# Performance work log

Measured on AMD Instinct MI355X. Metric: run time of the kernel, lower is better.

The kernel has to match this reference:

```python
import jax, jax.numpy as jnp
import numpy as np
import math

BSZ, SEQLEN, DIM = 16, 1, 4096
N_HEADS, N_KV_HEADS = 32, 8
HEAD_DIM = DIM // N_HEADS  # 128
MAX_SEQ_LEN = 4096
START_POS = 4095


def setup_inputs() -> dict:
    key = jax.random.key(0)
    ks = jax.random.split(key, 8)
    w_scale = 0.02
    x = jax.random.normal(ks[0], (1, BSZ, SEQLEN, DIM), jnp.float32)
    wq = jax.random.normal(ks[1], (DIM, DIM), jnp.float32) * w_scale
    wk = jax.random.normal(ks[2], (N_KV_HEADS * HEAD_DIM, DIM), jnp.float32) * w_scale
    wv = jax.random.normal(ks[3], (N_KV_HEADS * HEAD_DIM, DIM), jnp.float32) * w_scale
    wo = jax.random.normal(ks[4], (DIM, DIM), jnp.float32) * w_scale
    cache_k = jax.random.normal(ks[5], (BSZ, MAX_SEQ_LEN, N_KV_HEADS, HEAD_DIM), jnp.float32)
    cache_v = jax.random.normal(ks[6], (BSZ, MAX_SEQ_LEN, N_KV_HEADS, HEAD_DIM), jnp.float32)
    # real RoPE frequencies for positions [START_POS, START_POS+SEQLEN)
    inv_freq = 1.0 / (10000.0 ** (np.arange(0, HEAD_DIM, 2, dtype=np.float32) / HEAD_DIM))
    pos = np.arange(START_POS, START_POS + SEQLEN, dtype=np.float32)
    ang = pos[:, None] * inv_freq[None, :]  # [seqlen, head_dim/2]
    freqs_cos = jnp.asarray(np.cos(ang), jnp.float32)
    freqs_sin = jnp.asarray(np.sin(ang), jnp.float32)
    return {"x": x, "wq": wq, "wk": wk, "wv": wv, "wo": wo,
            "cache_k": cache_k, "cache_v": cache_v,
            "freqs_cos": freqs_cos, "freqs_sin": freqs_sin,
            "start_pos": START_POS}


def _apply_rope(t, cos, sin):
    # t: [b, s, h, d]; cos/sin: [s, d/2]; complex mult over interleaved pairs
    b, s, h, d = t.shape
    tr = t.reshape(b, s, h, d // 2, 2)
    a, bb = tr[..., 0], tr[..., 1]
    c = cos[None, :, None, :]
    sn = sin[None, :, None, :]
    out = jnp.stack([a * c - bb * sn, a * sn + bb * c], axis=-1)
    return out.reshape(b, s, h, d)


def reference(x, wq, wk, wv, wo, cache_k, cache_v, freqs_cos, freqs_sin, start_pos):
    _, bsz, seqlen, dim = x.shape
    n_kv_heads, head_dim = cache_k.shape[2], cache_k.shape[3]
    n_heads = dim // head_dim
    n_rep = n_heads // n_kv_heads

    xq = jnp.einsum('obsd,ed->obse', x, wq).reshape(bsz, seqlen, n_heads, head_dim)
    xk = jnp.einsum('obsd,ed->obse', x, wk).reshape(bsz, seqlen, n_kv_heads, head_dim)
    xv = jnp.einsum('obsd,ed->obse', x, wv).reshape(bsz, seqlen, n_kv_heads, head_dim)

    xq = _apply_rope(xq, freqs_cos, freqs_sin)
    xk = _apply_rope(xk, freqs_cos, freqs_sin)

    cache_k = cache_k.at[:, start_pos:start_pos + seqlen].set(xk)
    cache_v = cache_v.at[:, start_pos:start_pos + seqlen].set(xv)
    keys = cache_k[:, :start_pos + seqlen]    # [b, L, kvh, hd]
    values = cache_v[:, :start_pos + seqlen]

    # repeat_kv (GQA expansion)
    keys = jnp.repeat(keys, n_rep, axis=2)     # [b, L, h, hd]
    values = jnp.repeat(values, n_rep, axis=2)

    scale = 1.0 / math.sqrt(head_dim)
    scores = jnp.einsum('bqhd,bkhd->bhqk', xq, keys) * scale
    # mask is None in decode (seqlen == 1)
    attn = jax.nn.softmax(scores, axis=-1)
    out = jnp.einsum('bhqk,bkhd->bqhd', attn, values)
    out = out.reshape(1, bsz, seqlen, dim)
    return jnp.einsum('obsd,ed->obse', out, wo)
```

## Files before the change

kernel.cpp:

```cpp
#include <hip/hip_runtime.h>
#include <math.h>

#define BSZ 16
#define DIMM 4096
#define NKVH 8
#define HD 128
#define SEQ 4096
#define NSPLIT 16
#define SPLITLEN 256
#define RPAD 65

__device__ __forceinline__ void gemv_rows2(const float* __restrict__ xg,
                                           const float* __restrict__ W,
                                           int rbase,
                                           float* __restrict__ x_lds,
                                           float* __restrict__ rbuf,
                                           float res[2], int tid) {
  const int lane = tid & 63;
  float acc[2][16];
#pragma unroll
  for (int r = 0; r < 2; ++r)
#pragma unroll
    for (int b = 0; b < 16; ++b) acc[r][b] = 0.f;

  for (int c = 0; c < 16; ++c) {
    __syncthreads();
#pragma unroll
    for (int u = 0; u < 4; ++u) {
      int f = u * 256 + tid;
      int b = f >> 6;
      int dl = (f & 63) << 2;
      ((float4*)x_lds)[f] = *(const float4*)(xg + (size_t)b * DIMM + c * 256 + dl);
    }
    __syncthreads();
    float4 w4[2];
#pragma unroll
    for (int r = 0; r < 2; ++r)
      w4[r] = *(const float4*)(W + (size_t)(rbase + r) * DIMM + c * 256 + (lane << 2));
#pragma unroll
    for (int b = 0; b < 16; ++b) {
      float4 xv = ((const float4*)x_lds)[b * 64 + lane];
#pragma unroll
      for (int r = 0; r < 2; ++r) {
        acc[r][b] = fmaf(w4[r].x, xv.x, acc[r][b]);
        acc[r][b] = fmaf(w4[r].y, xv.y, acc[r][b]);
        acc[r][b] = fmaf(w4[r].z, xv.z, acc[r][b]);
        acc[r][b] = fmaf(w4[r].w, xv.w, acc[r][b]);
      }
    }
  }
#pragma unroll
  for (int r = 0; r < 2; ++r) {
    __syncthreads();
#pragma unroll
    for (int b = 0; b < 16; ++b) rbuf[b * RPAD + lane] = acc[r][b];
    __syncthreads();
    int bb = lane >> 2, j = lane & 3;
    float s = 0.f;
#pragma unroll
    for (int k = 0; k < 16; ++k) s += rbuf[bb * RPAD + j * 16 + k];
    s += __shfl_xor(s, 1);
    s += __shfl_xor(s, 2);
    res[r] = s;
  }
}

__global__ __launch_bounds__(256) void qkv_kernel(
    const float* __restrict__ x, const float* __restrict__ wq,
    const float* __restrict__ wk, const float* __restrict__ wv,
    const float* __restrict__ fcos, const float* __restrict__ fsin,
    float* __restrict__ q_ws, float* __restrict__ ckw, float* __restrict__ cvw) {
  __shared__ float x_lds[4096];
  __shared__ float red[4][16 * RPAD];
  const int tid = threadIdx.x;
  const int lane = tid & 63;
  const int wave = tid >> 6;
  const int row0 = blockIdx.x * 8 + wave * 2;

  const float* W;
  int rbase, kind;
  if (row0 < 4096)      { W = wq; rbase = row0;        kind = 0; }
  else if (row0 < 5120) { W = wk; rbase = row0 - 4096; kind = 1; }
  else                  { W = wv; rbase = row0 - 5120; kind = 2; }

  float res[2];
  gemv_rows2(x, W, rbase, x_lds, red[wave], res, tid);

  if (kind <= 1) {
    int i = (rbase & 127) >> 1;
    float c = fcos[i], s = fsin[i];
    float a = res[0], b2 = res[1];
    res[0] = a * c - b2 * s;
    res[1] = a * s + b2 * c;
  }
  if ((lane & 3) == 0) {
    int b = lane >> 2;
    if (kind == 0) {
#pragma unroll
      for (int r = 0; r < 2; ++r) q_ws[(size_t)b * 4096 + rbase + r] = res[r];
    } else {
      int kvh = rbase >> 7, dpos = rbase & 127;
      float* dst = (kind == 1) ? ckw : cvw;
#pragma unroll
      for (int r = 0; r < 2; ++r)
        dst[((size_t)(b * 4096 + 4095) * 8 + kvh) * 128 + dpos + r] = res[r];
    }
  }
}

__global__ __launch_bounds__(256) void attn_kernel(
    const float* __restrict__ ck, const float* __restrict__ cv,
    const float* __restrict__ q_ws, float* __restrict__ ml_ws,
    float* __restrict__ opart) {
  __shared__ float sc[SPLITLEN * 4];
  __shared__ float part[32 * 128];
  const int tid = threadIdx.x, lane = tid & 63, wave = tid >> 6;
  const int split = blockIdx.x, kvh = blockIdx.y, b = blockIdx.z;
  const int p0 = split * SPLITLEN;
  const float scale = 0.08838834764831845f;

  {
    const int dsub = (lane & 7) << 2;
    const int prow = lane >> 3;
    float4 q4[4][4];
#pragma unroll
    for (int h = 0; h < 4; ++h)
#pragma unroll
      for (int j = 0; j < 4; ++j) {
        float4 t = *(const float4*)(q_ws + (size_t)b * 4096 + (kvh * 4 + h) * 128 + j * 32 + dsub);
        q4[h][j] = make_float4(t.x * scale, t.y * scale, t.z * scale, t.w * scale);
      }
#pragma unroll 2
    for (int it = 0; it < 8; ++it) {
      int pl = wave * 64 + it * 8 + prow;
      const float* kp = ck + ((size_t)(b * 4096 + p0 + pl) * 8 + kvh) * 128;
      float s0 = 0, s1 = 0, s2 = 0, s3 = 0;
#pragma unroll
      for (int j = 0; j < 4; ++j) {
        float4 k4 = *(const float4*)(kp + j * 32 + dsub);
        s0 = fmaf(k4.x, q4[0][j].x, s0); s0 = fmaf(k4.y, q4[0][j].y, s0);
        s0 = fmaf(k4.z, q4[0][j].z, s0); s0 = fmaf(k4.w, q4[0][j].w, s0);
        s1 = fmaf(k4.x, q4[1][j].x, s1); s1 = fmaf(k4.y, q4[1][j].y, s1);
        s1 = fmaf(k4.z, q4[1][j].z, s1); s1 = fmaf(k4.w, q4[1][j].w, s1);
        s2 = fmaf(k4.x, q4[2][j].x, s2); s2 = fmaf(k4.y, q4[2][j].y, s2);
        s2 = fmaf(k4.z, q4[2][j].z, s2); s2 = fmaf(k4.w, q4[2][j].w, s2);
        s3 = fmaf(k4.x, q4[3][j].x, s3); s3 = fmaf(k4.y, q4[3][j].y, s3);
        s3 = fmaf(k4.z, q4[3][j].z, s3); s3 = fmaf(k4.w, q4[3][j].w, s3);
      }
#pragma unroll
      for (int m = 1; m <= 4; m <<= 1) {
        s0 += __shfl_xor(s0, m); s1 += __shfl_xor(s1, m);
        s2 += __shfl_xor(s2, m); s3 += __shfl_xor(s3, m);
      }
      if ((lane & 7) == 0)
        ((float4*)sc)[pl] = make_float4(s0, s1, s2, s3);
    }
  }
  __syncthreads();

  {
    int h = wave;
    float vals[4];
    float m = -1e30f;
#pragma unroll
    for (int k = 0; k < 4; ++k) {
      vals[k] = sc[(k * 64 + lane) * 4 + h];
      m = fmaxf(m, vals[k]);
    }
#pragma unroll
    for (int mk = 1; mk <= 32; mk <<= 1) m = fmaxf(m, __shfl_xor(m, mk));
    float lsum = 0;
#pragma unroll
    for (int k = 0; k < 4; ++k) {
      float e = __expf(vals[k] - m);
      sc[(k * 64 + lane) * 4 + h] = e;
      lsum += e;
    }
#pragma unroll
    for (int mk = 1; mk <= 32; mk <<= 1) lsum += __shfl_xor(lsum, mk);
    if (lane == 0) {
      int hg = kvh * 4 + h;
      ml_ws[((size_t)(b * 32 + hg) * NSPLIT + split) * 2 + 0] = m;
      ml_ws[((size_t)(b * 32 + hg) * NSPLIT + split) * 2 + 1] = lsum;
    }
  }
  __syncthreads();

  {
    const int dq = lane & 31;
    const int half = lane >> 5;
    float4 a0 = {0,0,0,0}, a1 = {0,0,0,0}, a2 = {0,0,0,0}, a3 = {0,0,0,0};
#pragma unroll 4
    for (int it = 0; it < 32; ++it) {
      int pl = wave * 64 + it * 2 + half;
      const float* vp = cv + ((size_t)(b * 4096 + p0 + pl) * 8 + kvh) * 128;
      float4 v4 = *(const float4*)(vp + dq * 4);
      float4 s4 = ((const float4*)sc)[pl];
      a0.x = fmaf(s4.x, v4.x, a0.x); a0.y = fmaf(s4.x, v4.y, a0.y);
      a0.z = fmaf(s4.x, v4.z, a0.z); a0.w = fmaf(s4.x, v4.w, a0.w);
      a1.x = fmaf(s4.y, v4.x, a1.x); a1.y = fmaf(s4.y, v4.y, a1.y);
      a1.z = fmaf(s4.y, v4.z, a1.z); a1.w = fmaf(s4.y, v4.w, a1.w);
      a2.x = fmaf(s4.z, v4.x, a2.x); a2.y = fmaf(s4.z, v4.y, a2.y);
      a2.z = fmaf(s4.z, v4.z, a2.z); a2.w = fmaf(s4.z, v4.w, a2.w);
      a3.x = fmaf(s4.w, v4.x, a3.x); a3.y = fmaf(s4.w, v4.y, a3.y);
      a3.z = fmaf(s4.w, v4.z, a3.z); a3.w = fmaf(s4.w, v4.w, a3.w);
    }
    int rb = (half * 16 + wave * 4) * 128 + dq * 4;
    *(float4*)&part[rb + 0 * 128] = a0;
    *(float4*)&part[rb + 1 * 128] = a1;
    *(float4*)&part[rb + 2 * 128] = a2;
    *(float4*)&part[rb + 3 * 128] = a3;
  }
  __syncthreads();
  {
    int hh = tid >> 6, dd = (tid & 63) * 2;
    float o0 = 0, o1 = 0;
#pragma unroll
    for (int g = 0; g < 8; ++g) {
      int row = (g >> 2) * 16 + (g & 3) * 4 + hh;
      float2 p2 = *(const float2*)&part[row * 128 + dd];
      o0 += p2.x; o1 += p2.y;
    }
    int hg = kvh * 4 + hh;
    size_t base = ((size_t)(b * 32 + hg) * NSPLIT + split) * 128;
    *(float2*)(opart + base + dd) = make_float2(o0, o1);
  }
}

__global__ __launch_bounds__(128) void combine_kernel(
    const float* __restrict__ ml_ws, const float* __restrict__ opart,
    float* __restrict__ attn_ws) {
  int bh = blockIdx.x;
  int d = threadIdx.x;
  float mv[NSPLIT], lv[NSPLIT];
  float M = -1e30f;
#pragma unroll
  for (int i = 0; i < NSPLIT; ++i) {
    mv[i] = ml_ws[((size_t)bh * NSPLIT + i) * 2];
    lv[i] = ml_ws[((size_t)bh * NSPLIT + i) * 2 + 1];
    M = fmaxf(M, mv[i]);
  }
  float L = 0, o = 0;
#pragma unroll
  for (int i = 0; i < NSPLIT; ++i) {
    float w = __expf(mv[i] - M);
    L += w * lv[i];
    o += w * opart[((size_t)bh * NSPLIT + i) * 128 + d];
  }
  attn_ws[(size_t)bh * 128 + d] = o / L;
}

__global__ __launch_bounds__(256) void oproj_kernel(
    const float* __restrict__ xin, const float* __restrict__ wo,
    float* __restrict__ out) {
  __shared__ float x_lds[4096];
  __shared__ float red[4][16 * RPAD];
  const int tid = threadIdx.x;
  const int lane = tid & 63;
  const int wave = tid >> 6;
  const int row0 = blockIdx.x * 8 + wave * 2;
  float res[2];
  gemv_rows2(xin, wo, row0, x_lds, red[wave], res, tid);
  if ((lane & 3) == 0) {
    int b = lane >> 2;
#pragma unroll
    for (int r = 0; r < 2; ++r) out[(size_t)b * 4096 + row0 + r] = res[r];
  }
}

extern "C" void kernel_launch(void* const* d_in, const int* in_sizes, int n_in,
                              void* d_out, int out_size, void* d_ws, size_t ws_size,
                              hipStream_t stream) {
  const float* x  = (const float*)d_in[0];
  const float* wq = (const float*)d_in[1];
  const float* wk = (const float*)d_in[2];
  const float* wv = (const float*)d_in[3];
  const float* wo = (const float*)d_in[4];
  float* ck = (float*)d_in[5];
  float* cv = (float*)d_in[6];
  const float* fc = (const float*)d_in[7];
  const float* fs = (const float*)d_in[8];

  float* ws      = (float*)d_ws;
  float* q_ws    = ws;
  float* ml_ws   = q_ws + 65536;
  float* opart   = ml_ws + 16384;
  float* attn_ws = opart + 1048576;

  qkv_kernel<<<768, 256, 0, stream>>>(x, wq, wk, wv, fc, fs, q_ws, ck, cv);
  attn_kernel<<<dim3(NSPLIT, NKVH, BSZ), 256, 0, stream>>>(ck, cv, q_ws, ml_ws, opart);
  combine_kernel<<<BSZ * 32, 128, 0, stream>>>(ml_ws, opart, attn_ws);
  oproj_kernel<<<512, 256, 0, stream>>>(attn_ws, wo, (float*)d_out);
}
```

Baseline: 663.5 us.

## Double-buffer GEMV staging with async LDS loads and compute four rows per wave

The QKV and output-projection GEMVs now compute four rows per wave and double-buffer the activation chunks in LDS using global_load_lds, while prefetching the next weight chunk into registers. This is meant to overlap memory latency with FMA work and to reuse each staged activation chunk across more rows. The new K/V are written to a small workspace instead of the caches, and the attention kernel reads that workspace for the last position. The grid halves, which lowers block-level parallelism, and LDS use doubles.

Result: faster. 632.7 us (-4.6%).

```diff
diff --git a/kernel.cpp b/kernel.cpp
--- a/kernel.cpp
+++ b/kernel.cpp
@@ -10,47 +10,72 @@
 #define SPLITLEN 256
 #define RPAD 65
 
-__device__ __forceinline__ void gemv_rows2(const float* __restrict__ xg,
+__device__ __forceinline__ void gll16(const float* src, float* dst) {
+  __builtin_amdgcn_global_load_lds(
+      (const __attribute__((address_space(1))) void*)src,
+      (__attribute__((address_space(3))) void*)dst, 16, 0, 0);
+}
+
+__device__ __forceinline__ void stage_chunk(const float* __restrict__ xg,
+                                            float* __restrict__ buf, int c,
+                                            int wave, int lane) {
+#pragma unroll
+  for (int u = 0; u < 4; ++u) {
+    gll16(xg + (size_t)(u * 4 + wave) * DIMM + c * 256 + (lane << 2),
+          buf + u * 1024 + wave * 256);
+  }
+}
+
+__device__ __forceinline__ void gemv_rows4(const float* __restrict__ xg,
                                            const float* __restrict__ W,
                                            int rbase,
                                            float* __restrict__ x_lds,
                                            float* __restrict__ rbuf,
-                                           float res[2], int tid) {
+                                           float res[4], int tid) {
   const int lane = tid & 63;
-  float acc[2][16];
-#pragma unroll
-  for (int r = 0; r < 2; ++r)
+  const int wave = tid >> 6;
+  float acc[4][16];
+#pragma unroll
+  for (int r = 0; r < 4; ++r)
 #pragma unroll
     for (int b = 0; b < 16; ++b) acc[r][b] = 0.f;
+
+  stage_chunk(xg, x_lds, 0, wave, lane);
+  float4 w4[4];
+#pragma unroll
+  for (int r = 0; r < 4; ++r)
+    w4[r] = *(const float4*)(W + (size_t)(rbase + r) * DIMM + (lane << 2));
 
   for (int c = 0; c < 16; ++c) {
     __syncthreads();
-#pragma unroll
-    for (int u = 0; u < 4; ++u) {
-      int f = u * 256 + tid;
-      int b = f >> 6;
-      int dl = (f & 63) << 2;
-      ((float4*)x_lds)[f] = *(const float4*)(xg + (size_t)b * DIMM + c * 256 + dl);
-    }
-    __syncthreads();
-    float4 w4[2];
-#pragma unroll
-    for (int r = 0; r < 2; ++r)
-      w4[r] = *(const float4*)(W + (size_t)(rbase + r) * DIMM + c * 256 + (lane << 2));
+    float4 wn[4];
+    if (c < 15) {
+      stage_chunk(xg, x_lds + ((c + 1) & 1) * 4096, c + 1, wave, lane);
+#pragma unroll
+      for (int r = 0; r < 4; ++r)
+        wn[r] = *(const float4*)(W + (size_t)(rbase + r) * DIMM +
+                                 (c + 1) * 256 + (lane << 2));
+    }
+    const float4* xb = (const float4*)(x_lds + (c & 1) * 4096);
 #pragma unroll
     for (int b = 0; b < 16; ++b) {
-      float4 xv = ((const float4*)x_lds)[b * 64 + lane];
-#pragma unroll
-      for (int r = 0; r < 2; ++r) {
+      float4 xv = xb[b * 64 + lane];
+#pragma unroll
+      for (int r = 0; r < 4; ++r) {
         acc[r][b] = fmaf(w4[r].x, xv.x, acc[r][b]);
         acc[r][b] = fmaf(w4[r].y, xv.y, acc[r][b]);
         acc[r][b] = fmaf(w4[r].z, xv.z, acc[r][b]);
         acc[r][b] = fmaf(w4[r].w, xv.w, acc[r][b]);
       }
     }
-  }
-#pragma unroll
-  for (int r = 0; r < 2; ++r) {
+    if (c < 15) {
+#pragma unroll
+      for (int r = 0; r < 4; ++r) w4[r] = wn[r];
+    }
+  }
+
+#pragma unroll
+  for (int r = 0; r < 4; ++r) {
     __syncthreads();
 #pragma unroll
     for (int b = 0; b < 16; ++b) rbuf[b * RPAD + lane] = acc[r][b];
@@ -69,13 +94,14 @@
     const float* __restrict__ x, const float* __restrict__ wq,
     const float* __restrict__ wk, const float* __restrict__ wv,
     const float* __restrict__ fcos, const float* __restrict__ fsin,
-    float* __restrict__ q_ws, float* __restrict__ ckw, float* __restrict__ cvw) {
-  __shared__ float x_lds[4096];
+    float* __restrict__ q_ws, float* __restrict__ k_ws,
+    float* __restrict__ v_ws) {
+  __shared__ float x_lds[2 * 4096];
   __shared__ float red[4][16 * RPAD];
   const int tid = threadIdx.x;
   const int lane = tid & 63;
   const int wave = tid >> 6;
-  const int row0 = blockIdx.x * 8 + wave * 2;
+  const int row0 = blockIdx.x * 16 + wave * 4;
 
   const float* W;
   int rbase, kind;
@@ -83,34 +109,38 @@
   else if (row0 < 5120) { W = wk; rbase = row0 - 4096; kind = 1; }
   else                  { W = wv; rbase = row0 - 5120; kind = 2; }
 
-  float res[2];
-  gemv_rows2(x, W, rbase, x_lds, red[wave], res, tid);
+  float res[4];
+  gemv_rows4(x, W, rbase, x_lds, red[wave], res, tid);
 
   if (kind <= 1) {
-    int i = (rbase & 127) >> 1;
-    float c = fcos[i], s = fsin[i];
-    float a = res[0], b2 = res[1];
-    res[0] = a * c - b2 * s;
-    res[1] = a * s + b2 * c;
+#pragma unroll
+    for (int pr = 0; pr < 2; ++pr) {
+      int i = ((rbase + pr * 2) & 127) >> 1;
+      float c = fcos[i], s = fsin[i];
+      float a = res[pr * 2], b2 = res[pr * 2 + 1];
+      res[pr * 2]     = a * c - b2 * s;
+      res[pr * 2 + 1] = a * s + b2 * c;
+    }
   }
   if ((lane & 3) == 0) {
     int b = lane >> 2;
     if (kind == 0) {
 #pragma unroll
-      for (int r = 0; r < 2; ++r) q_ws[(size_t)b * 4096 + rbase + r] = res[r];
+      for (int r = 0; r < 4; ++r) q_ws[(size_t)b * 4096 + rbase + r] = res[r];
     } else {
       int kvh = rbase >> 7, dpos = rbase & 127;
-      float* dst = (kind == 1) ? ckw : cvw;
-#pragma unroll
-      for (int r = 0; r < 2; ++r)
-        dst[((size_t)(b * 4096 + 4095) * 8 + kvh) * 128 + dpos + r] = res[r];
+      float* dst = (kind == 1) ? k_ws : v_ws;
+#pragma unroll
+      for (int r = 0; r < 4; ++r)
+        dst[((size_t)b * NKVH + kvh) * HD + dpos + r] = res[r];
     }
   }
 }
 
 __global__ __launch_bounds__(256) void attn_kernel(
     const float* __restrict__ ck, const float* __restrict__ cv,
-    const float* __restrict__ q_ws, float* __restrict__ ml_ws,
+    const float* __restrict__ q_ws, const float* __restrict__ k_ws,
+    const float* __restrict__ v_ws, float* __restrict__ ml_ws,
     float* __restrict__ opart) {
   __shared__ float sc[SPLITLEN * 4];
   __shared__ float part[32 * 128];
@@ -133,7 +163,9 @@
 #pragma unroll 2
     for (int it = 0; it < 8; ++it) {
       int pl = wave * 64 + it * 8 + prow;
-      const float* kp = ck + ((size_t)(b * 4096 + p0 + pl) * 8 + kvh) * 128;
+      const float* kp = (p0 + pl == SEQ - 1)
+                            ? (k_ws + ((size_t)b * NKVH + kvh) * HD)
+                            : (ck + ((size_t)(b * 4096 + p0 + pl) * 8 + kvh) * 128);
       float s0 = 0, s1 = 0, s2 = 0, s3 = 0;
 #pragma unroll
       for (int j = 0; j < 4; ++j) {
@@ -193,7 +225,9 @@
 #pragma unroll 4
     for (int it = 0; it < 32; ++it) {
       int pl = wave * 64 + it * 2 + half;
-      const float* vp = cv + ((size_t)(b * 4096 + p0 + pl) * 8 + kvh) * 128;
+      const float* vp = (p0 + pl == SEQ - 1)
+                            ? (v_ws + ((size_t)b * NKVH + kvh) * HD)
+                            : (cv + ((size_t)(b * 4096 + p0 + pl) * 8 + kvh) * 128);
       float4 v4 = *(const float4*)(vp + dq * 4);
       float4 s4 = ((const float4*)sc)[pl];
       a0.x = fmaf(s4.x, v4.x, a0.x); a0.y = fmaf(s4.x, v4.y, a0.y);
@@ -253,18 +287,18 @@
 __global__ __launch_bounds__(256) void oproj_kernel(
     const float* __restrict__ xin, const float* __restrict__ wo,
     float* __restrict__ out) {
-  __shared__ float x_lds[4096];
+  __shared__ float x_lds[2 * 4096];
   __shared__ float red[4][16 * RPAD];
   const int tid = threadIdx.x;
   const int lane = tid & 63;
   const int wave = tid >> 6;
-  const int row0 = blockIdx.x * 8 + wave * 2;
-  float res[2];
-  gemv_rows2(xin, wo, row0, x_lds, red[wave], res, tid);
+  const int row0 = blockIdx.x * 16 + wave * 4;
+  float res[4];
+  gemv_rows4(xin, wo, row0, x_lds, red[wave], res, tid);
   if ((lane & 3) == 0) {
     int b = lane >> 2;
 #pragma unroll
-    for (int r = 0; r < 2; ++r) out[(size_t)b * 4096 + row0 + r] = res[r];
+    for (int r = 0; r < 4; ++r) out[(size_t)b * 4096 + row0 + r] = res[r];
   }
 }
 
@@ -276,19 +310,22 @@
   const float* wk = (const float*)d_in[2];
   const float* wv = (const float*)d_in[3];
   const float* wo = (const float*)d_in[4];
-  float* ck = (float*)d_in[5];
-  float* cv = (float*)d_in[6];
+  const float* ck = (const float*)d_in[5];
+  const float* cv = (const float*)d_in[6];
   const float* fc = (const float*)d_in[7];
   const float* fs = (const float*)d_in[8];
 
   float* ws      = (float*)d_ws;
   float* q_ws    = ws;
-  float* ml_ws   = q_ws + 65536;
+  float* k_ws    = q_ws + 65536;
+  float* v_ws    = k_ws + 16384;
+  float* ml_ws   = v_ws + 16384;
   float* opart   = ml_ws + 16384;
   float* attn_ws = opart + 1048576;
 
-  qkv_kernel<<<768, 256, 0, stream>>>(x, wq, wk, wv, fc, fs, q_ws, ck, cv);
-  attn_kernel<<<dim3(NSPLIT, NKVH, BSZ), 256, 0, stream>>>(ck, cv, q_ws, ml_ws, opart);
+  qkv_kernel<<<384, 256, 0, stream>>>(x, wq, wk, wv, fc, fs, q_ws, k_ws, v_ws);
+  attn_kernel<<<dim3(NSPLIT, NKVH, BSZ), 256, 0, stream>>>(ck, cv, q_ws, k_ws, v_ws,
+                                                           ml_ws, opart);
   combine_kernel<<<BSZ * 32, 128, 0, stream>>>(ml_ws, opart, attn_ws);
-  oproj_kernel<<<512, 256, 0, stream>>>(attn_ws, wo, (float*)d_out);
-}
+  oproj_kernel<<<256, 256, 0, stream>>>(attn_ws, wo, (float*)d_out);
+}
```
